# Performance work log

Hardware: AMD Instinct MI355X
Metric: run time of the kernel (lower is better)

## Reference

```python
import jax, jax.numpy as jnp
import numpy as np


def _pairwise_sq(x, y):
    # squared euclidean distances [B,N,M] via gram trick (avoids [B,N,M,D] temp)
    x2 = jnp.sum(x * x, -1)[:, :, None]
    y2 = jnp.sum(y * y, -1)[:, None, :]
    return x2 + y2 - 2.0 * jnp.einsum('bnd,bmd->bnm', x, y)


def _dtw_dp(C):
    # Subsequence DTW accumulated-cost matrix. C: [N,M].
    # D[0,:] = C[0,:] (free start anywhere in y);
    # D[i,j] = C[i,j] + min(D[i-1,j], D[i-1,j-1], D[i,j-1]).
    # Within-row recurrence D[i,j] = min(a[j], D[i,j-1] + C[i,j]) with
    # a[j] = min(D[i-1,j], D[i-1,j-1]) + C[i,j] is a min-plus prefix scan:
    # D[i,j] = S[j] + cummin(a - S)[j], S = cumsum(C[i]).
    inf = jnp.asarray(jnp.inf, C.dtype)
    def row(Dprev, Crow):
        shifted = jnp.concatenate([jnp.full((1,), inf, C.dtype), Dprev[:-1]])
        a = jnp.minimum(Dprev, shifted) + Crow
        S = jnp.cumsum(Crow)
        D = S + jax.lax.cummin(a - S)
        return D, D
    _, Dr = jax.lax.scan(row, C[0], C[1:])
    return jnp.concatenate([C[0][None], Dr], 0)


def _backtrack(D):
    # Backtrack optimal subseq-DTW path from (N-1, argmin D[-1]) to row 0.
    # Returns, per x index i, the largest y index aligned to i on the path
    # (== last occurrence kept by dict(dtw_path) in the torch code).
    N, M = D.shape
    inf = jnp.asarray(jnp.inf, D.dtype)
    j0 = jnp.argmin(D[-1]).astype(jnp.int32)
    i0 = jnp.asarray(N - 1, jnp.int32)
    yl = jnp.zeros((N,), jnp.int32).at[i0].set(j0)
    def step(carry, _):
        i, j, yl = carry
        dd = jnp.where(j > 0, D[i - 1, j - 1], inf)
        du = D[i - 1, j]
        dl = jnp.where(j > 0, D[i, j - 1], inf)
        best = jnp.minimum(jnp.minimum(dd, du), dl)
        take_d = dd == best
        take_u = (~take_d) & (du == best)
        ni = jnp.where(take_d | take_u, i - 1, i)
        nj = jnp.where(take_d, j - 1, jnp.where(take_u, j, j - 1))
        active = i > 0
        ni = jnp.where(active, ni, i)
        nj = jnp.where(active, nj, j)
        yl = jnp.where(active, yl.at[ni].max(nj), yl)
        return (ni, nj, yl), None
    (_, _, yl), _ = jax.lax.scan(step, (i0, j0, yl), None, length=N + M)
    return yl


def setup_inputs() -> dict:
    key = jax.random.key(0)
    k0, k1, k2, k3 = jax.random.split(key, 4)
    B, N, M, D = 16, 1024, 4096, 64
    return {
        'x': jax.random.normal(k0, (B, N, D), jnp.float32),
        'y': jax.random.normal(k1, (B, M, D), jnp.float32),
        'x_t': jax.random.uniform(k2, (B, N), dtype=jnp.float32),
        'y_t': jax.random.uniform(k3, (B, M), dtype=jnp.float32),
    }


def reference(x, y, x_t, y_t):
    C = _pairwise_sq(x, y)                      # [B,N,M]
    D = jax.vmap(_dtw_dp)(C)                    # [B,N,M]
    # total path cost == DP optimum (sum of C along the optimal path)
    dtw_cost = jnp.min(D[:, -1, :], axis=-1)    # [B]
    y_last = jax.vmap(_backtrack)(jax.lax.stop_gradient(D))  # [B,N] int32
    w_ts = x_t                                  # path covers all x indices 0..N-1 in order
    w_vs = jnp.take_along_axis(y_t, y_last, axis=1)
    return dtw_cost, w_ts, w_vs
```

## Files before the change

### kernel.cpp

```cpp
#include <hip/hip_runtime.h>

#define B_ 16
#define N_ 1024
#define M_ 4096
#define D_ 64
#define SROWS_ (N_ + 63)
#define SROWSP_ (SROWS_ + 9)
#define SPAIR_ 544
#define TSB_ ((size_t)SPAIR_ * 128)
#define BTQ_ 96

__device__ __forceinline__ float finf() { return __builtin_inff(); }

__device__ __forceinline__ float wave_shr1(float x) {
  return __int_as_float(__builtin_amdgcn_update_dpp(
      0, __float_as_int(x), 0x138, 0xF, 0xF, false));
}
__device__ __forceinline__ float rdlane(float v, int l) {
  return __int_as_float(__builtin_amdgcn_readlane(__float_as_int(v), l));
}

__global__ void prep_kernel(const float* __restrict__ x,
                            const float* __restrict__ x_t,
                            float* __restrict__ x2,
                            float* __restrict__ w_ts_out) {
  int id = blockIdx.x * blockDim.x + threadIdx.x;
  const float4* xr = (const float4*)(x + (size_t)id * D_);
  float s = 0.f;
#pragma unroll
  for (int e = 0; e < D_ / 4; ++e) {
    float4 v = xr[e];
    s += v.x * v.x + v.y * v.y + v.z * v.z + v.w * v.w;
  }
  x2[id] = s;
  w_ts_out[id] = x_t[id];
}

__global__ __launch_bounds__(256) void gemm_kernel(
    const float* __restrict__ x, const float* __restrict__ y,
    const float* __restrict__ x2, float* __restrict__ Cs, int chunkBase) {
  const int b = blockIdx.z;
  const int tile = blockIdx.x;
  const int t = threadIdx.x;
  const int cg = t & 63;
  const int rg = t >> 6;
  const int ibeg = blockIdx.y * 32;
  float* CsT = Cs + (size_t)(b * 4 + tile) * SROWSP_ * 256;

  __shared__ float4 ylds[16 * 256];
  __shared__ float4 xlds[16 * 32];
  __shared__ float y2lds[256];

  {
    const int j = chunkBase + tile * 256 + t;
    const float4* yrow = (const float4*)(y + ((size_t)b * M_ + j) * D_);
    float4 yr[16];
#pragma unroll
    for (int e = 0; e < 16; ++e) yr[e] = yrow[e];
    float y2 = 0.f;
#pragma unroll
    for (int e = 0; e < 16; ++e)
      y2 += yr[e].x * yr[e].x + yr[e].y * yr[e].y + yr[e].z * yr[e].z +
            yr[e].w * yr[e].w;
    y2lds[t] = y2;
#pragma unroll
    for (int e = 0; e < 16; ++e) ylds[e * 256 + t] = yr[e];
  }
  if (t < 128) {
    const int row = t >> 2;
    const int part = t & 3;
    const float4* xr = (const float4*)(x + ((size_t)b * N_ + ibeg + row) * D_);
#pragma unroll
    for (int k = 0; k < 4; ++k) {
      const int e = part * 4 + k;
      xlds[e * 32 + row] = xr[e];
    }
  }
  __syncthreads();

  const int r0 = rg * 8;
  float acc[8][4];
#pragma unroll
  for (int r = 0; r < 8; ++r)
#pragma unroll
    for (int c = 0; c < 4; ++c) acc[r][c] = 0.f;

#pragma unroll
  for (int kb = 0; kb < 4; ++kb) {
    float4 yf[4][4];
#pragma unroll
    for (int c = 0; c < 4; ++c)
#pragma unroll
      for (int ee = 0; ee < 4; ++ee)
        yf[c][ee] = ylds[(kb * 4 + ee) * 256 + cg + 64 * c];
#pragma unroll
    for (int r = 0; r < 8; ++r) {
      float4 xv[4];
#pragma unroll
      for (int ee = 0; ee < 4; ++ee)
        xv[ee] = xlds[(kb * 4 + ee) * 32 + r0 + r];
#pragma unroll
      for (int ee = 0; ee < 4; ++ee) {
#pragma unroll
        for (int c = 0; c < 4; ++c) {
          acc[r][c] += xv[ee].x * yf[c][ee].x + xv[ee].y * yf[c][ee].y +
                       xv[ee].z * yf[c][ee].z + xv[ee].w * yf[c][ee].w;
        }
      }
    }
  }

#pragma unroll
  for (int r = 0; r < 8; ++r) {
    const int i = ibeg + r0 + r;
    const float xx = x2[b * N_ + i];
#pragma unroll
    for (int c = 0; c < 4; ++c) {
      const int ct = cg + 64 * c;
      const int l = ct >> 2;
      CsT[(size_t)(i + l) * 256 + ct] = xx + y2lds[ct] - 2.f * acc[r][c];
    }
  }
}

__global__ __launch_bounds__(256) void dtw_dp(
    const float* __restrict__ Cs, unsigned char* __restrict__ dec,
    const float* __restrict__ carryIn, float* __restrict__ carryOut,
    float* __restrict__ partV, int* __restrict__ partJ,
    int chunk, int hasCarry) {
  const int b = blockIdx.x;
  const int t = threadIdx.x;
  const int lane = t & 63;
  const int W = t >> 6;

  __shared__ float ring[3][1024];
  __shared__ float cring[1024];
  __shared__ int prog[3];
  __shared__ float redV[4];
  __shared__ int redJ[4];
  volatile int* vProg = prog;

  if (t < 3) prog[t] = -1;
  const float* cIn = carryIn + b * N_;
  if (hasCarry) ((float4*)cring)[t] = ((const float4*)cIn)[t];
  __syncthreads();

  const float INF = finf();
  const float* loadP = Cs + (size_t)(b * 4 + W) * SROWSP_ * 256;
  const int tileG = chunk * 4 + W;
  unsigned short* decP =
      (unsigned short*)(dec + (size_t)(b * 16 + tileG) * TSB_) + lane;
  float* carryB = carryOut + b * N_;
  const int jbase = tileG * 256 + lane * 4;

  float4 cc0 = ((const float4*)(loadP + 0 * 256))[lane];
  float4 cc1 = ((const float4*)(loadP + 1 * 256))[lane];
  float4 cc2 = ((const float4*)(loadP + 2 * 256))[lane];
  float4 cc3 = ((const float4*)(loadP + 3 * 256))[lane];
  float4 cc4 = ((const float4*)(loadP + 4 * 256))[lane];
  float4 cc5 = ((const float4*)(loadP + 5 * 256))[lane];
  float4 cc6 = ((const float4*)(loadP + 6 * 256))[lane];
  float4 cc7 = ((const float4*)(loadP + 7 * 256))[lane];
  loadP += 8 * 256;

  float edgeVec = INF, lvPrev = INF;
  float up0 = 0.f, up1 = 0.f, up2 = 0.f, up3 = 0.f;
  float dpp1 = INF, dpp2 = INF;
  float fin0 = INF, fin1 = INF, fin2 = INF, fin3 = INF;
  float ebuf[8];

#define BLOCKHEAD()                                                           \
  {                                                                           \
    if (W > 0) {                                                              \
      if (sb < N_) {                                                          \
        const int tgt = sb + 7;                                               \
        while (vProg[W - 1] < tgt) {}                                         \
        asm volatile("" ::: "memory");                                        \
        lvPrev = rdlane(edgeVec, 7);                                          \
        edgeVec = ring[W - 1][(sb + lane) & 1023];                            \
      }                                                                       \
    } else if (hasCarry) {                                                    \
      lvPrev = rdlane(edgeVec, 7);                                            \
      if (sb < N_) edgeVec = cring[(sb + lane) & 1023];                       \
    }                                                                         \
  }

#define DPSTEP(KK, CCV, ROW0, FIN)                                            \
  {                                                                           \
    const float lv = rdlane(edgeVec, (KK));                                   \
    const float left = (lane == 0) ? lv : dpp1;                               \
    const float diag = (lane == 0) ? lvPrev : dpp2;                           \
    lvPrev = lv;                                                              \
    float m0 = fminf(up0, left);                                              \
    float bv0 = fminf(diag, m0);                                              \
    unsigned int pk = (diag <= m0) ? 0u : ((up0 <= left) ? 1u : 2u);          \
    if (ROW0) bv0 = (sb + (KK) == lane) ? 0.f : bv0;                          \
    const float D0 = CCV.x + bv0;                                             \
    float m1 = fminf(up1, D0);                                                \
    float bv1 = fminf(up0, m1);                                               \
    pk |= ((up0 <= m1) ? 0u : ((up1 <= D0) ? 1u : 2u)) << 2;                  \
    if (ROW0) bv1 = (sb + (KK) == lane) ? 0.f : bv1;                          \
    const float D1 = CCV.y + bv1;                                             \
    float m2 = fminf(up2, D1);                                                \
    float bv2 = fminf(up1, m2);                                               \
    pk |= ((up1 <= m2) ? 0u : ((up2 <= D1) ? 1u : 2u)) << 4;                  \
    if (ROW0) bv2 = (sb + (KK) == lane) ? 0.f : bv2;                          \
    const float D2 = CCV.z + bv2;                                             \
    float m3 = fminf(up3, D2);                                                \
    float bv3 = fminf(up2, m3);                                               \
    pk |= ((up2 <= m3) ? 0u : ((up3 <= D2) ? 1u : 2u)) << 6;                  \
    if (ROW0) bv3 = (sb + (KK) == lane) ? 0.f : bv3;                          \
    const float D3 = CCV.w + bv3;                                             \
    ebuf[(KK)] = D3;                                                          \
    if ((KK) & 1) {                                                           \
      pk16 |= pk << 8;                                                        \
      decP[((KK) >> 1) * 64] = (unsigned short)pk16;                          \
    } else {                                                                  \
      pk16 = pk;                                                              \
    }                                                                         \
    if (FIN) {                                                                \
      const bool lr = (sb + (KK) == 1023 + lane);                             \
      fin0 = lr ? D0 : fin0; fin1 = lr ? D1 : fin1;                           \
      fin2 = lr ? D2 : fin2; fin3 = lr ? D3 : fin3;                           \
    }                                                                         \
    const float sh = wave_shr1(D3);                                           \
    dpp2 = dpp1; dpp1 = sh;                                                   \
    up0 = D0; up1 = D1; up2 = D2; up3 = D3;                                   \
    CCV = ((const float4*)(loadP + (KK) * 256))[lane];                        \
  }

#define BLOCKEND()                                                            \
  {                                                                           \
    const int r0 = sb - 63;                                                   \
    if (W < 3) {                                                              \
      if (lane == 63 && r0 > -8 && r0 < N_) {                                 \
        _Pragma("unroll") for (int k = 0; k < 8; ++k) {                       \
          const int r = r0 + k;                                               \
          if ((unsigned)r < (unsigned)N_) ring[W][r] = ebuf[k];               \
        }                                                                     \
        __builtin_amdgcn_s_waitcnt(0xC07F);                                   \
        vProg[W] = r0 + 7;                                                    \
      }                                                                       \
    } else if (chunk < 3) {                                                   \
      if (lane == 63 && r0 > -8 && r0 < N_) {                                 \
        _Pragma("unroll") for (int k = 0; k < 8; ++k) {                       \
          const int r = r0 + k;                                               \
          if ((unsigned)r < (unsigned)N_) carryB[r] = ebuf[k];                \
        }                                                                     \
      }                                                                       \
    }                                                                         \
    loadP += 8 * 256;                                                         \
    decP += 256;                                                              \
  }

#define STEP8(R0, FN)                                                         \
  DPSTEP(0, cc0, R0, FN) DPSTEP(1, cc1, R0, FN) DPSTEP(2, cc2, R0, FN)        \
  DPSTEP(3, cc3, R0, FN) DPSTEP(4, cc4, R0, FN) DPSTEP(5, cc5, R0, FN)        \
  DPSTEP(6, cc6, R0, FN) DPSTEP(7, cc7, R0, FN)

  int sb = 0;
  for (; sb < 64; sb += 8) {
    BLOCKHEAD();
    unsigned int pk16;
    STEP8(1, 0)
    BLOCKEND();
  }
  for (; sb < 1016; sb += 8) {
    BLOCKHEAD();
    unsigned int pk16;
    STEP8(0, 0)
    BLOCKEND();
  }
  for (; sb < 1088; sb += 8) {
    BLOCKHEAD();
    unsigned int pk16;
    STEP8(0, 1)
    BLOCKEND();
  }
#undef DPSTEP
#undef STEP8
#undef BLOCKHEAD
#undef BLOCKEND

  float mv = fin0; int mj = jbase;
  if (fin1 < mv) { mv = fin1; mj = jbase + 1; }
  if (fin2 < mv) { mv = fin2; mj = jbase + 2; }
  if (fin3 < mv) { mv = fin3; mj = jbase + 3; }
#pragma unroll
  for (int off = 32; off > 0; off >>= 1) {
    const float ov = __shfl_down(mv, off);
    const int oj = __shfl_down(mj, off);
    if (ov < mv || (ov == mv && oj < mj)) { mv = ov; mj = oj; }
  }
  if (lane == 0) { redV[W] = mv; redJ[W] = mj; }
  __syncthreads();
  if (t == 0) {
    float bm = redV[0]; int bj = redJ[0];
#pragma unroll
    for (int w = 1; w < 4; ++w)
      if (redV[w] < bm) { bm = redV[w]; bj = redJ[w]; }
    partV[b * 4 + chunk] = bm;
    partJ[b * 4 + chunk] = bj;
  }
}

__global__ __launch_bounds__(64) void backtrack_kernel(
    const unsigned char* __restrict__ dec, const float* __restrict__ partV,
    const int* __restrict__ partJ, int nch, const float* __restrict__ y_t,
    float* __restrict__ w_vs, float* __restrict__ cost_out) {
  const int b = blockIdx.x;
  const int lane = threadIdx.x;
  __shared__ unsigned int stage[3 * 2048];
  __shared__ unsigned short tab[64][BTQ_ * 4 + 2];
  __shared__ int st_i, st_j;
  __shared__ int jrow[65];
  const unsigned char* db = dec + (size_t)b * 16 * TSB_;
  const float* yt = y_t + b * M_;
  float* wv = w_vs + b * N_;

  if (lane == 0) {
    float bc = finf(); int bj = 0;
    for (int c = 0; c < nch; ++c) {
      const float v = partV[b * nch + c];
      const int j = partJ[b * nch + c];
      if (v < bc) { bc = v; bj = j; }
    }
    cost_out[b] = bc;
    st_i = N_ - 1;
    st_j = bj;
    wv[N_ - 1] = yt[bj];
  }
  for (;;) {
    __syncthreads();
    const int i = st_i, j = st_j;
    if (i <= 0) break;
    const int qj = j >> 2;
    int qlo = qj - (BTQ_ - 1);
    if (qlo < 0) qlo = 0;
    const int Tbase = qlo >> 6;
    int plo = (i - 63) >> 1;
    if (plo < 0) plo = 0;

#pragma unroll
    for (int tt = 0; tt < 3; ++tt) {
      int T = Tbase + tt;
      if (T > 15) T = 15;
      const uint4* src =
          (const uint4*)(db + (size_t)T * TSB_ + (size_t)plo * 128);
#pragma unroll
      for (int v = 0; v < 8; ++v) {
        const int wb = tt * 8192 + (v * 64 + lane) * 16;
        const int sw = wb ^ (((wb >> 7) & 7) << 4);
        *(uint4*)((char*)stage + sw) = src[v * 64 + lane];
      }
    }
    __syncthreads();

    const int r = i - lane;
    if (r >= 1) {
      const unsigned char* sb8 = (const unsigned char*)stage;
      unsigned char wr[BTQ_];
#pragma unroll
      for (int k = 0; k < BTQ_; ++k) {
        const int q = qlo + k;
        const int tt = (q >> 6) - Tbase;
        const int l = q & 63;
        const int s = r + l;
        int idx = tt * 8192 + ((s >> 1) - plo) * 128 + l * 2 + (s & 1);
        idx ^= ((idx >> 7) & 7) << 4;
        wr[k] = sb8[idx];
      }
      unsigned short run = 0xFFFF;
#pragma unroll
      for (int k = 0; k < BTQ_; ++k) {
        const unsigned int byte = wr[k];
#pragma unroll
        for (int cs = 0; cs < 4; ++cs) {
          const unsigned int code = (byte >> (2 * cs)) & 3u;
          const int c = 4 * k + cs;
          const unsigned short v =
              (code != 2u) ? (unsigned short)((c << 2) | code) : run;
          tab[lane][c] = v;
          run = v;
        }
      }
    }
    __syncthreads();
    if (lane == 0) {
      const int base = qlo << 2;
      int rr = i, cj = j;
      while (rr >= 1 && (i - rr) < 64) {
        const int l = i - rr;
        const int c = cj - base;
        if (c < 0) break;
        const unsigned short v = tab[l][c];
        if (v == 0xFFFF) { cj = base - 1; break; }
        const int e = v >> 2;
        const int ce = v & 3;
        cj = base + e - (ce == 0 ? 1 : 0);
        --rr;
        jrow[i - rr] = cj;
      }
      st_i = rr;
      st_j = cj;
    }
    __syncthreads();
    const int cnt = i - st_i;
    if (lane < cnt) wv[i - 1 - lane] = yt[jrow[lane + 1]];
  }
}

extern "C" void kernel_launch(void* const* d_in, const int* in_sizes, int n_in,
                              void* d_out, int out_size, void* d_ws, size_t ws_size,
                              hipStream_t stream) {
  const float* x = (const float*)d_in[0];
  const float* y = (const float*)d_in[1];
  const float* x_t = (const float*)d_in[2];
  const float* y_t = (const float*)d_in[3];

  float* out_cost = (float*)d_out;
  float* out_wts = out_cost + B_;
  float* out_wvs = out_wts + B_ * N_;

  const size_t csBytes = (size_t)B_ * 4 * SROWSP_ * 256 * 4;
  const size_t decBytes = (size_t)B_ * 16 * TSB_;
  const size_t x2Bytes = (size_t)B_ * N_ * 4;

  char* ws = (char*)d_ws;
  float* Cs = (float*)ws;
  unsigned char* dec = (unsigned char*)(ws + csBytes);
  float* x2 = (float*)(ws + csBytes + decBytes);
  float* carryA = (float*)(ws + csBytes + decBytes + x2Bytes);
  float* carryB = carryA + B_ * N_;
  float* partV = carryB + B_ * N_;
  int* partJ = (int*)(partV + B_ * 4);

  prep_kernel<<<dim3((B_ * N_) / 256), 256, 0, stream>>>(x, x_t, x2, out_wts);

  float* cbuf[2] = {carryA, carryB};
  for (int c = 0; c < 4; ++c) {
    gemm_kernel<<<dim3(4, N_ / 32, B_), 256, 0, stream>>>(x, y, x2, Cs,
                                                          c * 1024);
    const float* cin = cbuf[(c + 1) & 1];
    float* cout = cbuf[c & 1];
    dtw_dp<<<dim3(B_), 256, 0, stream>>>(Cs, dec, cin, cout, partV, partJ, c,
                                         c > 0 ? 1 : 0);
  }

  backtrack_kernel<<<dim3(B_), 64, 0, stream>>>(dec, partV, partJ, 4, y_t,
                                                out_wvs, out_cost);
}
```

Measured before the change: 1.173 ms.

## Double DP register prefetch depth and process 128 backtrack rows per round

The DP kernel now prefetches 16 rows of cost tiles into registers instead of 8, alternating two 8-row halves so loads for the next block overlap the current block. The cost buffer row padding is increased to match. The backtrack kernel stages twice as many decision rows and builds a 128-row lookup table per iteration, so fewer serial rounds with their barriers and global loads are needed. In exchange it uses more VGPRs in the DP kernel, which may reduce occupancy, and more LDS and per-round work in the backtrack.

```diff
diff --git a/kernel.cpp b/kernel.cpp
--- a/kernel.cpp
+++ b/kernel.cpp
@@ -5,10 +5,11 @@
 #define M_ 4096
 #define D_ 64
 #define SROWS_ (N_ + 63)
-#define SROWSP_ (SROWS_ + 9)
+#define SROWSP_ (SROWS_ + 17)
 #define SPAIR_ 544
 #define TSB_ ((size_t)SPAIR_ * 128)
 #define BTQ_ 96
+#define BTROWS_ 128
 
 __device__ __forceinline__ float finf() { return __builtin_inff(); }
 
@@ -161,7 +162,15 @@
   float4 cc5 = ((const float4*)(loadP + 5 * 256))[lane];
   float4 cc6 = ((const float4*)(loadP + 6 * 256))[lane];
   float4 cc7 = ((const float4*)(loadP + 7 * 256))[lane];
-  loadP += 8 * 256;
+  float4 cc8 = ((const float4*)(loadP + 8 * 256))[lane];
+  float4 cc9 = ((const float4*)(loadP + 9 * 256))[lane];
+  float4 cc10 = ((const float4*)(loadP + 10 * 256))[lane];
+  float4 cc11 = ((const float4*)(loadP + 11 * 256))[lane];
+  float4 cc12 = ((const float4*)(loadP + 12 * 256))[lane];
+  float4 cc13 = ((const float4*)(loadP + 13 * 256))[lane];
+  float4 cc14 = ((const float4*)(loadP + 14 * 256))[lane];
+  float4 cc15 = ((const float4*)(loadP + 15 * 256))[lane];
+  loadP += 16 * 256;
 
   float edgeVec = INF, lvPrev = INF;
   float up0 = 0.f, up1 = 0.f, up2 = 0.f, up3 = 0.f;
@@ -253,32 +262,49 @@
     decP += 256;                                                              \
   }
 
-#define STEP8(R0, FN)                                                         \
+#define STEP8L(R0, FN)                                                        \
   DPSTEP(0, cc0, R0, FN) DPSTEP(1, cc1, R0, FN) DPSTEP(2, cc2, R0, FN)        \
   DPSTEP(3, cc3, R0, FN) DPSTEP(4, cc4, R0, FN) DPSTEP(5, cc5, R0, FN)        \
   DPSTEP(6, cc6, R0, FN) DPSTEP(7, cc7, R0, FN)
+#define STEP8H(R0, FN)                                                        \
+  DPSTEP(0, cc8, R0, FN) DPSTEP(1, cc9, R0, FN) DPSTEP(2, cc10, R0, FN)       \
+  DPSTEP(3, cc11, R0, FN) DPSTEP(4, cc12, R0, FN) DPSTEP(5, cc13, R0, FN)     \
+  DPSTEP(6, cc14, R0, FN) DPSTEP(7, cc15, R0, FN)
 
   int sb = 0;
-  for (; sb < 64; sb += 8) {
-    BLOCKHEAD();
-    unsigned int pk16;
-    STEP8(1, 0)
-    BLOCKEND();
-  }
-  for (; sb < 1016; sb += 8) {
-    BLOCKHEAD();
-    unsigned int pk16;
-    STEP8(0, 0)
-    BLOCKEND();
-  }
-  for (; sb < 1088; sb += 8) {
-    BLOCKHEAD();
-    unsigned int pk16;
-    STEP8(0, 1)
-    BLOCKEND();
+  for (; sb < 64;) {
+    BLOCKHEAD();
+    { unsigned int pk16; STEP8L(1, 0) }
+    BLOCKEND();
+    sb += 8;
+    BLOCKHEAD();
+    { unsigned int pk16; STEP8H(1, 0) }
+    BLOCKEND();
+    sb += 8;
+  }
+  for (; sb < 1008;) {
+    BLOCKHEAD();
+    { unsigned int pk16; STEP8L(0, 0) }
+    BLOCKEND();
+    sb += 8;
+    BLOCKHEAD();
+    { unsigned int pk16; STEP8H(0, 0) }
+    BLOCKEND();
+    sb += 8;
+  }
+  for (; sb < 1088;) {
+    BLOCKHEAD();
+    { unsigned int pk16; STEP8L(0, 1) }
+    BLOCKEND();
+    sb += 8;
+    BLOCKHEAD();
+    { unsigned int pk16; STEP8H(0, 1) }
+    BLOCKEND();
+    sb += 8;
   }
 #undef DPSTEP
-#undef STEP8
+#undef STEP8L
+#undef STEP8H
 #undef BLOCKHEAD
 #undef BLOCKEND
 
@@ -310,10 +336,10 @@
     float* __restrict__ w_vs, float* __restrict__ cost_out) {
   const int b = blockIdx.x;
   const int lane = threadIdx.x;
-  __shared__ unsigned int stage[3 * 2048];
-  __shared__ unsigned short tab[64][BTQ_ * 4 + 2];
+  __shared__ unsigned int stage[3 * 3072];
+  __shared__ unsigned short tab[BTROWS_][BTQ_ * 4 + 2];
   __shared__ int st_i, st_j;
-  __shared__ int jrow[65];
+  __shared__ int jrow[BTROWS_ + 1];
   const unsigned char* db = dec + (size_t)b * 16 * TSB_;
   const float* yt = y_t + b * M_;
   float* wv = w_vs + b * N_;
@@ -338,7 +364,7 @@
     int qlo = qj - (BTQ_ - 1);
     if (qlo < 0) qlo = 0;
     const int Tbase = qlo >> 6;
-    int plo = (i - 63) >> 1;
+    int plo = (i - 127) >> 1;
     if (plo < 0) plo = 0;
 
 #pragma unroll
@@ -348,40 +374,44 @@
       const uint4* src =
           (const uint4*)(db + (size_t)T * TSB_ + (size_t)plo * 128);
 #pragma unroll
-      for (int v = 0; v < 8; ++v) {
-        const int wb = tt * 8192 + (v * 64 + lane) * 16;
+      for (int v = 0; v < 12; ++v) {
+        const int wb = tt * 12288 + (v * 64 + lane) * 16;
         const int sw = wb ^ (((wb >> 7) & 7) << 4);
         *(uint4*)((char*)stage + sw) = src[v * 64 + lane];
       }
     }
     __syncthreads();
 
-    const int r = i - lane;
-    if (r >= 1) {
-      const unsigned char* sb8 = (const unsigned char*)stage;
-      unsigned char wr[BTQ_];
-#pragma unroll
-      for (int k = 0; k < BTQ_; ++k) {
-        const int q = qlo + k;
-        const int tt = (q >> 6) - Tbase;
-        const int l = q & 63;
-        const int s = r + l;
-        int idx = tt * 8192 + ((s >> 1) - plo) * 128 + l * 2 + (s & 1);
-        idx ^= ((idx >> 7) & 7) << 4;
-        wr[k] = sb8[idx];
-      }
-      unsigned short run = 0xFFFF;
-#pragma unroll
-      for (int k = 0; k < BTQ_; ++k) {
-        const unsigned int byte = wr[k];
-#pragma unroll
-        for (int cs = 0; cs < 4; ++cs) {
-          const unsigned int code = (byte >> (2 * cs)) & 3u;
-          const int c = 4 * k + cs;
-          const unsigned short v =
-              (code != 2u) ? (unsigned short)((c << 2) | code) : run;
-          tab[lane][c] = v;
-          run = v;
+    const unsigned char* sb8 = (const unsigned char*)stage;
+#pragma unroll
+    for (int half = 0; half < 2; ++half) {
+      const int r = i - lane - half * 64;
+      if (r >= 1) {
+        unsigned char wr[BTQ_];
+#pragma unroll
+        for (int k = 0; k < BTQ_; ++k) {
+          const int q = qlo + k;
+          const int tt = (q >> 6) - Tbase;
+          const int l = q & 63;
+          const int s = r + l;
+          int idx = tt * 12288 + ((s >> 1) - plo) * 128 + l * 2 + (s & 1);
+          idx ^= ((idx >> 7) & 7) << 4;
+          wr[k] = sb8[idx];
+        }
+        unsigned short run = 0xFFFF;
+        const int tr = lane + half * 64;
+#pragma unroll
+        for (int k = 0; k < BTQ_; ++k) {
+          const unsigned int byte = wr[k];
+#pragma unroll
+          for (int cs = 0; cs < 4; ++cs) {
+            const unsigned int code = (byte >> (2 * cs)) & 3u;
+            const int c = 4 * k + cs;
+            const unsigned short v =
+                (code != 2u) ? (unsigned short)((c << 2) | code) : run;
+            tab[tr][c] = v;
+            run = v;
+          }
         }
       }
     }
@@ -389,7 +419,7 @@
     if (lane == 0) {
       const int base = qlo << 2;
       int rr = i, cj = j;
-      while (rr >= 1 && (i - rr) < 64) {
+      while (rr >= 1 && (i - rr) < BTROWS_) {
         const int l = i - rr;
         const int c = cj - base;
         if (c < 0) break;
@@ -407,6 +437,10 @@
     __syncthreads();
     const int cnt = i - st_i;
     if (lane < cnt) wv[i - 1 - lane] = yt[jrow[lane + 1]];
+    {
+      const int l2 = lane + 64;
+      if (l2 < cnt) wv[i - 1 - l2] = yt[jrow[l2 + 1]];
+    }
   }
 }
 
```

Measured after the change: 1.186 ms. No clear change (+1.1%).

## Batch inter-wave sync per 64 rows and double backtrack rows per iteration

Applied to the files above, without the earlier changes.

The DP wavefront kernel now waits on the upstream wave's progress counter once per 64-row superblock instead of every 8 rows, reading lanes of the edge vector by offset, which cuts spin-wait and ring-load overhead. The backtrack kernel processes 128 rows per iteration instead of 64, using larger shared staging and two half passes per lane, so fewer sync rounds are needed. The predecessor-code comparisons are also simplified to compare against the final min. Waiting for more rows adds pipeline latency between waves and uses more LDS, which may lower occupancy. The row padding constant is bumped to match.

```diff
diff --git a/kernel.cpp b/kernel.cpp
--- a/kernel.cpp
+++ b/kernel.cpp
@@ -5,10 +5,11 @@
 #define M_ 4096
 #define D_ 64
 #define SROWS_ (N_ + 63)
-#define SROWSP_ (SROWS_ + 9)
+#define SROWSP_ (SROWS_ + 17)
 #define SPAIR_ 544
 #define TSB_ ((size_t)SPAIR_ * 128)
 #define BTQ_ 96
+#define BTROWS_ 128
 
 __device__ __forceinline__ float finf() { return __builtin_inff(); }
 
@@ -169,46 +170,40 @@
   float fin0 = INF, fin1 = INF, fin2 = INF, fin3 = INF;
   float ebuf[8];
 
-#define BLOCKHEAD()                                                           \
+#define SUPERHEAD()                                                           \
   {                                                                           \
     if (W > 0) {                                                              \
       if (sb < N_) {                                                          \
-        const int tgt = sb + 7;                                               \
+        const int tgt = sb + 63;                                              \
         while (vProg[W - 1] < tgt) {}                                         \
         asm volatile("" ::: "memory");                                        \
-        lvPrev = rdlane(edgeVec, 7);                                          \
         edgeVec = ring[W - 1][(sb + lane) & 1023];                            \
       }                                                                       \
     } else if (hasCarry) {                                                    \
-      lvPrev = rdlane(edgeVec, 7);                                            \
       if (sb < N_) edgeVec = cring[(sb + lane) & 1023];                       \
     }                                                                         \
   }
 
 #define DPSTEP(KK, CCV, ROW0, FIN)                                            \
   {                                                                           \
-    const float lv = rdlane(edgeVec, (KK));                                   \
+    const float lv = rdlane(edgeVec, u0 + (KK));                              \
     const float left = (lane == 0) ? lv : dpp1;                               \
     const float diag = (lane == 0) ? lvPrev : dpp2;                           \
     lvPrev = lv;                                                              \
-    float m0 = fminf(up0, left);                                              \
-    float bv0 = fminf(diag, m0);                                              \
-    unsigned int pk = (diag <= m0) ? 0u : ((up0 <= left) ? 1u : 2u);          \
+    float bv0 = fminf(diag, fminf(up0, left));                                \
+    unsigned int pk = (diag <= bv0) ? 0u : ((up0 <= bv0) ? 1u : 2u);          \
     if (ROW0) bv0 = (sb + (KK) == lane) ? 0.f : bv0;                          \
     const float D0 = CCV.x + bv0;                                             \
-    float m1 = fminf(up1, D0);                                                \
-    float bv1 = fminf(up0, m1);                                               \
-    pk |= ((up0 <= m1) ? 0u : ((up1 <= D0) ? 1u : 2u)) << 2;                  \
+    float bv1 = fminf(up0, fminf(up1, D0));                                   \
+    pk |= (up0 <= bv1) ? 0u : ((up1 <= bv1) ? 4u : 8u);                       \
     if (ROW0) bv1 = (sb + (KK) == lane) ? 0.f : bv1;                          \
     const float D1 = CCV.y + bv1;                                             \
-    float m2 = fminf(up2, D1);                                                \
-    float bv2 = fminf(up1, m2);                                               \
-    pk |= ((up1 <= m2) ? 0u : ((up2 <= D1) ? 1u : 2u)) << 4;                  \
+    float bv2 = fminf(up1, fminf(up2, D1));                                   \
+    pk |= (up1 <= bv2) ? 0u : ((up2 <= bv2) ? 16u : 32u);                     \
     if (ROW0) bv2 = (sb + (KK) == lane) ? 0.f : bv2;                          \
     const float D2 = CCV.z + bv2;                                             \
-    float m3 = fminf(up3, D2);                                                \
-    float bv3 = fminf(up2, m3);                                               \
-    pk |= ((up2 <= m3) ? 0u : ((up3 <= D2) ? 1u : 2u)) << 6;                  \
+    float bv3 = fminf(up2, fminf(up3, D2));                                   \
+    pk |= (up2 <= bv3) ? 0u : ((up3 <= bv3) ? 64u : 128u);                    \
     if (ROW0) bv3 = (sb + (KK) == lane) ? 0.f : bv3;                          \
     const float D3 = CCV.w + bv3;                                             \
     ebuf[(KK)] = D3;                                                          \
@@ -259,27 +254,39 @@
   DPSTEP(6, cc6, R0, FN) DPSTEP(7, cc7, R0, FN)
 
   int sb = 0;
-  for (; sb < 64; sb += 8) {
-    BLOCKHEAD();
-    unsigned int pk16;
-    STEP8(1, 0)
-    BLOCKEND();
-  }
-  for (; sb < 1016; sb += 8) {
-    BLOCKHEAD();
-    unsigned int pk16;
-    STEP8(0, 0)
-    BLOCKEND();
-  }
-  for (; sb < 1088; sb += 8) {
-    BLOCKHEAD();
-    unsigned int pk16;
-    STEP8(0, 1)
-    BLOCKEND();
+  {
+    SUPERHEAD();
+    for (int blk = 0; blk < 8; ++blk) {
+      const int u0 = blk * 8;
+      unsigned int pk16;
+      STEP8(1, 0)
+      BLOCKEND();
+      sb += 8;
+    }
+  }
+  for (int sup = 1; sup < 15; ++sup) {
+    SUPERHEAD();
+    for (int blk = 0; blk < 8; ++blk) {
+      const int u0 = blk * 8;
+      unsigned int pk16;
+      STEP8(0, 0)
+      BLOCKEND();
+      sb += 8;
+    }
+  }
+  for (int sup = 15; sup < 17; ++sup) {
+    SUPERHEAD();
+    for (int blk = 0; blk < 8; ++blk) {
+      const int u0 = blk * 8;
+      unsigned int pk16;
+      STEP8(0, 1)
+      BLOCKEND();
+      sb += 8;
+    }
   }
 #undef DPSTEP
 #undef STEP8
-#undef BLOCKHEAD
+#undef SUPERHEAD
 #undef BLOCKEND
 
   float mv = fin0; int mj = jbase;
@@ -310,10 +317,10 @@
     float* __restrict__ w_vs, float* __restrict__ cost_out) {
   const int b = blockIdx.x;
   const int lane = threadIdx.x;
-  __shared__ unsigned int stage[3 * 2048];
-  __shared__ unsigned short tab[64][BTQ_ * 4 + 2];
+  __shared__ unsigned int stage[3 * 3072];
+  __shared__ unsigned short tab[BTROWS_][BTQ_ * 4 + 2];
   __shared__ int st_i, st_j;
-  __shared__ int jrow[65];
+  __shared__ int jrow[BTROWS_ + 1];
   const unsigned char* db = dec + (size_t)b * 16 * TSB_;
   const float* yt = y_t + b * M_;
   float* wv = w_vs + b * N_;
@@ -338,7 +345,7 @@
     int qlo = qj - (BTQ_ - 1);
     if (qlo < 0) qlo = 0;
     const int Tbase = qlo >> 6;
-    int plo = (i - 63) >> 1;
+    int plo = (i - 127) >> 1;
     if (plo < 0) plo = 0;
 
 #pragma unroll
@@ -348,40 +355,44 @@
       const uint4* src =
           (const uint4*)(db + (size_t)T * TSB_ + (size_t)plo * 128);
 #pragma unroll
-      for (int v = 0; v < 8; ++v) {
-        const int wb = tt * 8192 + (v * 64 + lane) * 16;
+      for (int v = 0; v < 12; ++v) {
+        const int wb = tt * 12288 + (v * 64 + lane) * 16;
         const int sw = wb ^ (((wb >> 7) & 7) << 4);
         *(uint4*)((char*)stage + sw) = src[v * 64 + lane];
       }
     }
     __syncthreads();
 
-    const int r = i - lane;
-    if (r >= 1) {
-      const unsigned char* sb8 = (const unsigned char*)stage;
-      unsigned char wr[BTQ_];
-#pragma unroll
-      for (int k = 0; k < BTQ_; ++k) {
-        const int q = qlo + k;
-        const int tt = (q >> 6) - Tbase;
-        const int l = q & 63;
-        const int s = r + l;
-        int idx = tt * 8192 + ((s >> 1) - plo) * 128 + l * 2 + (s & 1);
-        idx ^= ((idx >> 7) & 7) << 4;
-        wr[k] = sb8[idx];
-      }
-      unsigned short run = 0xFFFF;
-#pragma unroll
-      for (int k = 0; k < BTQ_; ++k) {
-        const unsigned int byte = wr[k];
-#pragma unroll
-        for (int cs = 0; cs < 4; ++cs) {
-          const unsigned int code = (byte >> (2 * cs)) & 3u;
-          const int c = 4 * k + cs;
-          const unsigned short v =
-              (code != 2u) ? (unsigned short)((c << 2) | code) : run;
-          tab[lane][c] = v;
-          run = v;
+    const unsigned char* sb8 = (const unsigned char*)stage;
+#pragma unroll
+    for (int half = 0; half < 2; ++half) {
+      const int r = i - lane - half * 64;
+      if (r >= 1) {
+        unsigned char wr[BTQ_];
+#pragma unroll
+        for (int k = 0; k < BTQ_; ++k) {
+          const int q = qlo + k;
+          const int tt = (q >> 6) - Tbase;
+          const int l = q & 63;
+          const int s = r + l;
+          int idx = tt * 12288 + ((s >> 1) - plo) * 128 + l * 2 + (s & 1);
+          idx ^= ((idx >> 7) & 7) << 4;
+          wr[k] = sb8[idx];
+        }
+        unsigned short run = 0xFFFF;
+        const int tr = lane + half * 64;
+#pragma unroll
+        for (int k = 0; k < BTQ_; ++k) {
+          const unsigned int byte = wr[k];
+#pragma unroll
+          for (int cs = 0; cs < 4; ++cs) {
+            const unsigned int code = (byte >> (2 * cs)) & 3u;
+            const int c = 4 * k + cs;
+            const unsigned short v =
+                (code != 2u) ? (unsigned short)((c << 2) | code) : run;
+            tab[tr][c] = v;
+            run = v;
+          }
         }
       }
     }
@@ -389,7 +400,7 @@
     if (lane == 0) {
       const int base = qlo << 2;
       int rr = i, cj = j;
-      while (rr >= 1 && (i - rr) < 64) {
+      while (rr >= 1 && (i - rr) < BTROWS_) {
         const int l = i - rr;
         const int c = cj - base;
         if (c < 0) break;
@@ -407,6 +418,10 @@
     __syncthreads();
     const int cnt = i - st_i;
     if (lane < cnt) wv[i - 1 - lane] = yt[jrow[lane + 1]];
+    {
+      const int l2 = lane + 64;
+      if (l2 < cnt) wv[i - 1 - l2] = yt[jrow[l2 + 1]];
+    }
   }
 }
 
```

New measurement: 1.258 ms. 7.2% more time.
